# Optimization experiments

Hardware: AMD Instinct MI355X
Metric: run time of the kernel (lower is better)

Reference implementation:

```python
import jax, jax.numpy as jnp
import numpy as np

NUM_HEADS = 12
HEAD_DIM = 64


def setup_inputs() -> dict:
    key = jax.random.key(0)
    ks = jax.random.split(key, 4)
    B, T, C = 2, 2048, 768
    x = jax.random.normal(ks[0], (B, T, C), dtype=jnp.float32)
    attention_mask = jnp.ones((B, 1, 1, T), dtype=jnp.int32)
    W_attn = jax.random.normal(ks[1], (C, 3 * C), dtype=jnp.float32) * 0.02
    b_attn = jnp.zeros((3 * C,), dtype=jnp.float32)
    W_proj = jax.random.normal(ks[2], (C, C), dtype=jnp.float32) * 0.02
    b_proj = jnp.zeros((C,), dtype=jnp.float32)
    return {"x": x, "attention_mask": attention_mask, "W_attn": W_attn,
            "b_attn": b_attn, "W_proj": W_proj, "b_proj": b_proj}


def reference(x, attention_mask, W_attn, b_attn, W_proj, b_proj):
    B, T, C = x.shape
    H, D = NUM_HEADS, HEAD_DIM
    # c_attn (Conv1D): y = x @ W + b -> [B, T, 3C]
    qkv = x @ W_attn + b_attn
    q, k, v = jnp.split(qkv, 3, axis=-1)
    # [B, T, C] -> [B, H, T, D]
    q = q.reshape(B, T, H, D).transpose(0, 2, 1, 3)
    k = k.reshape(B, T, H, D).transpose(0, 2, 1, 3)
    v = v.reshape(B, T, H, D).transpose(0, 2, 1, 3)
    scores = jnp.einsum('bhqd,bhkd->bhqk', q, k) / jnp.sqrt(jnp.float32(D))
    causal = jnp.tril(jnp.ones((T, T), dtype=bool))[None, None]  # [1,1,T,T]
    mask_value = jnp.finfo(scores.dtype).min
    scores = jnp.where(causal, scores, mask_value)
    scores = jnp.where(attention_mask == 0, -jnp.inf, scores)
    probs = jax.nn.softmax(scores, axis=-1)
    attn_out = jnp.einsum('bhqk,bhkd->bhqd', probs, v)
    attn_out = attn_out.transpose(0, 2, 1, 3).reshape(B, T, C)
    return attn_out @ W_proj + b_proj
```

## Files before the change

### kernel.cpp

```cpp
#include <hip/hip_runtime.h>

typedef __attribute__((ext_vector_type(8))) short bf16x8;
typedef __attribute__((ext_vector_type(4))) float f32x4;
typedef __attribute__((ext_vector_type(16))) float f32x16;

#define MFMA16(a, b, c) __builtin_amdgcn_mfma_f32_16x16x32_bf16(a, b, c, 0, 0, 0)
#define MFMA32(a, b, c) __builtin_amdgcn_mfma_f32_32x32x16_bf16(a, b, c, 0, 0, 0)
#define LOG2E 1.4426950408889634f
#define MB2 46.16624868f

#define BB 2
#define TT 2048
#define CC 768
#define HH 12
#define DD 64
#define MM (BB * TT)
#define N1 (3 * CC)
#define BH_STRIDE 131072

static __device__ __forceinline__ unsigned short f2bf(float f) {
  union { float f; unsigned u; } v; v.f = f;
  unsigned r = (v.u + 0x7FFFu + ((v.u >> 16) & 1u)) >> 16;
  return (unsigned short)r;
}

static __device__ __forceinline__ float bf2f(unsigned short s) {
  union { unsigned u; float f; } v; v.u = ((unsigned)s) << 16;
  return v.f;
}

static __device__ __forceinline__ unsigned cvt_pk_bf16(float lo, float hi) {
  unsigned r;
  asm("v_cvt_pk_bf16_f32 %0, %1, %2" : "=v"(r) : "v"(lo), "v"(hi));
  return r;
}

static __device__ __forceinline__ void gload_lds16(const void* g, void* l) {
  __builtin_amdgcn_global_load_lds(
      (const __attribute__((address_space(1))) void*)g,
      (__attribute__((address_space(3))) void*)l, 16, 0, 0);
}

#define PREP_CVT 3072
#define PREP_TR1 1728
#define PREP_TR2 576
__global__ __launch_bounds__(256) void k_prep(
    const float* __restrict__ x, unsigned short* __restrict__ Xb,
    const float* __restrict__ Wa, unsigned short* __restrict__ WaT,
    const float* __restrict__ Wp, unsigned short* __restrict__ WpT,
    const int* __restrict__ mask, unsigned int* __restrict__ mb) {
  __shared__ float tile[32][33];
  const int bid = blockIdx.x;
  const int tid = threadIdx.x;
  if (bid < PREP_CVT) {
    const int i = bid * 256 + tid;
    float4 v = reinterpret_cast<const float4*>(x)[i];
    ushort4 r;
    r.x = f2bf(v.x); r.y = f2bf(v.y); r.z = f2bf(v.z); r.w = f2bf(v.w);
    reinterpret_cast<ushort4*>(Xb)[i] = r;
  } else if (bid < PREP_CVT + PREP_TR1 + PREP_TR2) {
    const bool first = bid < PREP_CVT + PREP_TR1;
    const int b = first ? bid - PREP_CVT : bid - PREP_CVT - PREP_TR1;
    const int nb = first ? 72 : 24;
    const int N = first ? N1 : CC;
    const float* W = first ? Wa : Wp;
    unsigned short* Wt = first ? WaT : WpT;
    const int n0 = (b % nb) * 32, k0 = (b / nb) * 32;
    const int tx = tid & 31, ty = tid >> 5;
#pragma unroll
    for (int i = 0; i < 4; ++i)
      tile[ty + i * 8][tx] = W[(size_t)(k0 + ty + i * 8) * N + n0 + tx];
    __syncthreads();
#pragma unroll
    for (int i = 0; i < 4; ++i)
      Wt[(size_t)(n0 + ty + i * 8) * CC + k0 + tx] = f2bf(tile[tx][ty + i * 8]);
  } else {
    if (tid < 128) {
      unsigned bits = 0;
      const int* p = mask + tid * 32;
#pragma unroll
      for (int j = 0; j < 32; ++j) bits |= (p[j] != 0 ? 1u : 0u) << j;
      mb[tid] = bits;
    }
  }
}

template <int MODE, int BN>
__global__ __launch_bounds__(256) void k_gemm(
    const unsigned short* __restrict__ A, const unsigned short* __restrict__ Bt,
    const float* __restrict__ bias, float* __restrict__ Cout, int N, int K,
    unsigned short* __restrict__ Qb, unsigned short* __restrict__ Kb,
    unsigned short* __restrict__ Vt) {
  constexpr int NI = BN / 32;
  __shared__ __align__(16) unsigned short As[3][128 * 32];
  __shared__ __align__(16) unsigned short Bs[3][BN * 32];
  const int tid = threadIdx.x;
  const int lane = tid & 63;
  const int wid = tid >> 6;
  const int l15 = lane & 15, l4 = lane >> 4;
  const int wr = wid >> 1, wc = wid & 1;
  const int brow = blockIdx.x * 128, bcol = blockIdx.y * BN;

  f32x4 acc[4][NI] = {};

  const int srow = tid >> 2;
  const int usrc = (tid & 3) ^ ((tid >> 3) & 3);
  const unsigned short* gA0 = A + (size_t)(brow + srow) * K + usrc * 8;
  const unsigned short* gA1 = gA0 + (size_t)64 * K;
  const unsigned short* gB0 = Bt + (size_t)(bcol + srow) * K + usrc * 8;
  const unsigned short* gB1 = (BN == 128) ? gB0 + (size_t)64 * K : gB0;
  const int dslot = tid * 8;

  const int NT = K / 32;

#define STAGE(t, buf)                                       \
  do {                                                      \
    const int ko = (t) * 32;                                \
    gload_lds16(gA0 + ko, &As[buf][dslot]);                 \
    gload_lds16(gA1 + ko, &As[buf][dslot + 2048]);          \
    gload_lds16(gB0 + ko, &Bs[buf][dslot]);                 \
    if (BN == 128) gload_lds16(gB1 + ko, &Bs[buf][dslot + 2048]); \
  } while (0)

  const int swz = (l4 ^ ((l15 >> 1) & 3)) * 8;
  const int arow = wr * 64 + l15;
  const int brow2 = wc * (BN / 2) + l15;

  STAGE(0, 0);
  STAGE(1, 1);

  int cur = 0;
  for (int t = 0; t < NT - 1; ++t) {
    if (BN == 128) asm volatile("s_waitcnt vmcnt(4)" ::: "memory");
    else           asm volatile("s_waitcnt vmcnt(3)" ::: "memory");
    __builtin_amdgcn_s_barrier();
    if (t + 2 < NT) {
      int nb = cur + 2; if (nb >= 3) nb -= 3;
      STAGE(t + 2, nb);
    }
    bf16x8 af[4], bfr[NI];
#pragma unroll
    for (int mi = 0; mi < 4; ++mi)
      af[mi] = *reinterpret_cast<const bf16x8*>(&As[cur][(arow + mi * 16) * 32 + swz]);
#pragma unroll
    for (int ni = 0; ni < NI; ++ni)
      bfr[ni] = *reinterpret_cast<const bf16x8*>(&Bs[cur][(brow2 + ni * 16) * 32 + swz]);
#pragma unroll
    for (int mi = 0; mi < 4; ++mi)
#pragma unroll
      for (int ni = 0; ni < NI; ++ni)
        acc[mi][ni] = MFMA16(af[mi], bfr[ni], acc[mi][ni]);
    cur = (cur == 2) ? 0 : cur + 1;
  }
  asm volatile("s_waitcnt vmcnt(0)" ::: "memory");
  __builtin_amdgcn_s_barrier();
  {
    bf16x8 af[4], bfr[NI];
#pragma unroll
    for (int mi = 0; mi < 4; ++mi)
      af[mi] = *reinterpret_cast<const bf16x8*>(&As[cur][(arow + mi * 16) * 32 + swz]);
#pragma unroll
    for (int ni = 0; ni < NI; ++ni)
      bfr[ni] = *reinterpret_cast<const bf16x8*>(&Bs[cur][(brow2 + ni * 16) * 32 + swz]);
#pragma unroll
    for (int mi = 0; mi < 4; ++mi)
#pragma unroll
      for (int ni = 0; ni < NI; ++ni)
        acc[mi][ni] = MFMA16(af[mi], bfr[ni], acc[mi][ni]);
  }
#undef STAGE

#pragma unroll
  for (int mi = 0; mi < 4; ++mi) {
    const int m0 = brow + wr * 64 + mi * 16 + l4 * 4;
#pragma unroll
    for (int ni = 0; ni < NI; ++ni) {
      const int n = bcol + wc * (BN / 2) + ni * 16 + l15;
      const float bv = bias[n];
      if (MODE == 0) {
#pragma unroll
        for (int r = 0; r < 4; ++r)
          Cout[(size_t)(m0 + r) * N + n] = acc[mi][ni][r] + bv;
      } else {
        const int sec = n / CC;
        const int nn = n - sec * CC;
        const int hh = nn >> 6, d = nn & 63;
        const int b = m0 >> 11;
        const int t0 = m0 & 2047;
        const size_t hbase = (size_t)(b * HH + hh) * BH_STRIDE;
        if (sec == 0) {
#pragma unroll
          for (int r = 0; r < 4; ++r) {
            const int t = t0 + r;
            Qb[hbase + ((t >> 5) * 4 + (d >> 4)) * 512 + (t & 31) * 16 + (d & 15)] =
                f2bf((acc[mi][ni][r] + bv) * 0.125f);
          }
        } else if (sec == 1) {
#pragma unroll
          for (int r = 0; r < 4; ++r) {
            const int t = t0 + r;
            Kb[hbase + ((t >> 5) * 4 + (d >> 4)) * 512 + (t & 31) * 16 + (d & 15)] =
                f2bf(acc[mi][ni][r] + bv);
          }
        } else {
          ushort4 pk;
          pk.x = f2bf(acc[mi][ni][0] + bv);
          pk.y = f2bf(acc[mi][ni][1] + bv);
          pk.z = f2bf(acc[mi][ni][2] + bv);
          pk.w = f2bf(acc[mi][ni][3] + bv);
          *reinterpret_cast<ushort4*>(
              &Vt[hbase + ((t0 >> 6) * 4 + ((t0 >> 4) & 3)) * 1024 + d * 16 + (t0 & 15)]) = pk;
        }
      }
    }
  }
}

__device__ __forceinline__ void loadk(bf16x8 (&dst)[2][4], const unsigned short* Kh,
                                      int kv0, int lo) {
  const unsigned short* kp = Kh + (kv0 >> 5) * 2048 + lo;
#pragma unroll
  for (int kg = 0; kg < 2; ++kg)
#pragma unroll
    for (int dg = 0; dg < 4; ++dg)
      dst[kg][dg] = *reinterpret_cast<const bf16x8*>(&kp[kg * 2048 + dg * 512]);
}

__device__ __forceinline__ void attn_tile(
    int kv0, const bf16x8 (&kf)[2][4], uint2 mb, const bf16x8 (&qf)[4],
    const unsigned short* __restrict__ Vh, int q0, int l31, int h, int lo,
    f32x16& o0, f32x16& o1, float& lrow) {
  const unsigned short* vp = Vh + (kv0 >> 6) * 4096 + lo;
  bf16x8 vf0[4], vf1[4];
#pragma unroll
  for (int kc = 0; kc < 4; ++kc) {
    vf0[kc] = *reinterpret_cast<const bf16x8*>(&vp[kc * 1024]);
    vf1[kc] = *reinterpret_cast<const bf16x8*>(&vp[kc * 1024 + 512]);
  }

  f32x16 s0 = {}, s1 = {};
  __builtin_amdgcn_s_setprio(1);
#pragma unroll
  for (int dg = 0; dg < 4; ++dg) s0 = MFMA32(kf[0][dg], qf[dg], s0);
#pragma unroll
  for (int dg = 0; dg < 4; ++dg) s1 = MFMA32(kf[1][dg], qf[dg], s1);
  __builtin_amdgcn_s_setprio(0);

  if ((mb.x & mb.y) != 0xffffffffu) {
#pragma unroll
    for (int r = 0; r < 16; ++r) {
      const int ki = (r & 3) + 8 * (r >> 2) + 4 * h;
      if (!((mb.x >> ki) & 1u)) s0[r] = -1e30f;
      if (!((mb.y >> ki) & 1u)) s1[r] = -1e30f;
    }
  }
  if (kv0 + 63 > q0) {
    const int q = q0 + l31;
#pragma unroll
    for (int r = 0; r < 16; ++r) {
      const int ki = kv0 + (r & 3) + 8 * (r >> 2) + 4 * h;
      if (ki > q) s0[r] = -1e30f;
      if (ki + 32 > q) s1[r] = -1e30f;
    }
  }

#pragma unroll
  for (int r = 0; r < 16; ++r) {
    s0[r] = __builtin_amdgcn_exp2f(__builtin_fmaf(s0[r], LOG2E, -MB2));
    s1[r] = __builtin_amdgcn_exp2f(__builtin_fmaf(s1[r], LOG2E, -MB2));
  }
  float ts[8];
#pragma unroll
  for (int r = 0; r < 8; ++r)
    ts[r] = (s0[2 * r] + s0[2 * r + 1]) + (s1[2 * r] + s1[2 * r + 1]);
  float ps = ((ts[0] + ts[1]) + (ts[2] + ts[3])) + ((ts[4] + ts[5]) + (ts[6] + ts[7]));
  ps += __shfl_xor(ps, 32);
  lrow += ps;

  unsigned pk0[4][2], pk1[4][2];
#pragma unroll
  for (int m = 0; m < 4; ++m)
#pragma unroll
    for (int j = 0; j < 2; ++j) {
      pk0[m][j] = cvt_pk_bf16(s0[4 * m + 2 * j], s0[4 * m + 2 * j + 1]);
      pk1[m][j] = cvt_pk_bf16(s1[4 * m + 2 * j], s1[4 * m + 2 * j + 1]);
    }

#pragma unroll
  for (int kc = 0; kc < 4; ++kc) {
    const unsigned (&pkk)[4][2] = (kc < 2) ? pk0 : pk1;
    const int c1 = (kc & 1) * 2;
    const unsigned v0 = h ? pkk[c1][0] : pkk[c1 + 1][0];
    const unsigned v1 = h ? pkk[c1][1] : pkk[c1 + 1][1];
    const unsigned r0 = (unsigned)__shfl_xor((int)v0, 32);
    const unsigned r1 = (unsigned)__shfl_xor((int)v1, 32);
    union { unsigned u[4]; bf16x8 v; } af;
    af.u[0] = h ? r0 : pkk[c1][0];
    af.u[1] = h ? r1 : pkk[c1][1];
    af.u[2] = h ? pkk[c1 + 1][0] : r0;
    af.u[3] = h ? pkk[c1 + 1][1] : r1;
    __builtin_amdgcn_s_setprio(1);
    o0 = MFMA32(af.v, vf0[kc], o0);
    o1 = MFMA32(af.v, vf1[kc], o1);
    __builtin_amdgcn_s_setprio(0);
  }
}

__global__ __launch_bounds__(256, 2) void k_attn(
    const unsigned short* __restrict__ Q, const unsigned short* __restrict__ Kb,
    const unsigned short* __restrict__ Vt, const unsigned int* __restrict__ mbits,
    unsigned short* __restrict__ pO, float* __restrict__ pL,
    unsigned short* __restrict__ AO) {
  const int tid = threadIdx.x;
  const int lane = tid & 63;
  const int w = tid >> 6;
  const int l31 = lane & 31;
  const int h = lane >> 5;
  const int lo = l31 * 16 + h * 8;
  const int f = blockIdx.x;
  const int xcd = f & 7;
  const int i = f >> 3;
  const int hl = i % 3;
  const int j = i / 3;
  const int bh = xcd * 3 + hl;
  int g, c;
  if (j < 16)      { g = 15 - (j >> 2); c = j & 3; }
  else if (j < 28) { const int u = j - 16; g = 11 - u / 3; c = u % 3; }
  else if (j < 36) { const int u = j - 28; g = 7 - (u >> 1); c = u & 1; }
  else             { g = 3 - (j - 36); c = 0; }
  const int qb = 4 * g + w;
  int cb;
  if (qb < 16)      cb = qb;
  else if (qb < 32) cb = 16 + 2 * (qb - 16);
  else if (qb < 48) cb = 48 + 3 * (qb - 32);
  else              cb = 96 + 4 * (qb - 48);
  const int pidx = bh * 160 + cb + c;

  const int b = bh / HH;
  const int hd = bh - b * HH;
  const int q0 = qb * 32;
  const int nt = qb / 2 + 1;
  const int t0 = c * 8;
  const int t1 = (t0 + 8 < nt) ? t0 + 8 : nt;

  const unsigned short* Qh = Q + (size_t)bh * BH_STRIDE;
  const unsigned short* Kh = Kb + (size_t)bh * BH_STRIDE;
  const unsigned short* Vh = Vt + (size_t)bh * BH_STRIDE;
  const unsigned int* mbp = mbits + b * 64;

  bf16x8 qf[4];
  {
    const unsigned short* qp = Qh + (q0 >> 5) * 2048 + lo;
#pragma unroll
    for (int dg = 0; dg < 4; ++dg)
      qf[dg] = *reinterpret_cast<const bf16x8*>(&qp[dg * 512]);
  }

  f32x16 o0 = {}, o1 = {};
  float lrow = 0.f;

  bf16x8 kfA[2][4], kfB[2][4];
  uint2 mbA, mbB;
  loadk(kfA, Kh, t0 * 64, lo);
  mbA = *reinterpret_cast<const uint2*>(&mbp[t0 * 2]);

  int t = t0;
  while (true) {
    if (t + 1 < t1) {
      loadk(kfB, Kh, (t + 1) * 64, lo);
      mbB = *reinterpret_cast<const uint2*>(&mbp[(t + 1) * 2]);
    }
    attn_tile(t * 64, kfA, mbA, qf, Vh, q0, l31, h, lo, o0, o1, lrow);
    ++t; if (t >= t1) break;
    if (t + 1 < t1) {
      loadk(kfA, Kh, (t + 1) * 64, lo);
      mbA = *reinterpret_cast<const uint2*>(&mbp[(t + 1) * 2]);
    }
    attn_tile(t * 64, kfB, mbB, qf, Vh, q0, l31, h, lo, o0, o1, lrow);
    ++t; if (t >= t1) break;
  }

  if (t0 == 0 && t1 == nt) {
    const float rl = 1.0f / lrow;
#pragma unroll
    for (int r = 0; r < 16; ++r) {
      const int crow = (r & 3) + 8 * (r >> 2) + 4 * h;
      const float rb = __shfl(rl, crow);
      const size_t base = (size_t)(b * TT + q0 + crow) * CC + hd * DD;
      AO[base + l31] = f2bf(o0[r] * rb);
      AO[base + 32 + l31] = f2bf(o1[r] * rb);
    }
  } else {
    unsigned short* po = pO + (size_t)pidx * 2048;
#pragma unroll
    for (int r = 0; r < 16; ++r) {
      const int crow = (r & 3) + 8 * (r >> 2) + 4 * h;
      po[crow * 64 + l31] = f2bf(o0[r]);
      po[crow * 64 + 32 + l31] = f2bf(o1[r]);
    }
    if (lane < 32) {
      pL[pidx * 32 + lane] = lrow;
    }
  }
}

__global__ __launch_bounds__(256) void k_merge(
    const unsigned short* __restrict__ pO, const float* __restrict__ pL,
    unsigned short* __restrict__ AO) {
  const int qb = 16 + blockIdx.x, bh = blockIdx.y;
  const int b = bh / HH, hd = bh - b * HH;
  const int nt = qb / 2 + 1;
  const int nch = (nt + 7) >> 3;
  int cb;
  if (qb < 32)      cb = 16 + 2 * (qb - 16);
  else if (qb < 48) cb = 48 + 3 * (qb - 32);
  else              cb = 96 + 4 * (qb - 48);
  const int p0 = bh * 160 + cb;

  const int q = threadIdx.x >> 3;
  const int d0 = (threadIdx.x & 7) * 8;

  float lst = 0.f;
#pragma unroll
  for (int c = 0; c < 4; ++c)
    if (c < nch) lst += pL[(p0 + c) * 32 + q];
  const float inv = 1.0f / lst;

  float acc[8] = {};
#pragma unroll
  for (int c = 0; c < 4; ++c) {
    if (c < nch) {
      const unsigned short* po = pO + ((size_t)(p0 + c) * 32 + q) * 64 + d0;
      union { uint4 v; unsigned short u[8]; } rd;
      rd.v = *reinterpret_cast<const uint4*>(po);
#pragma unroll
      for (int jj = 0; jj < 8; ++jj) acc[jj] += bf2f(rd.u[jj]);
    }
  }
  union { unsigned short u[8]; uint4 v; } ov;
#pragma unroll
  for (int jj = 0; jj < 8; ++jj) ov.u[jj] = f2bf(acc[jj] * inv);
  *reinterpret_cast<uint4*>(&AO[(size_t)(b * TT + qb * 32 + q) * CC + hd * DD + d0]) = ov.v;
}

extern "C" void kernel_launch(void* const* d_in, const int* in_sizes, int n_in,
                              void* d_out, int out_size, void* d_ws, size_t ws_size,
                              hipStream_t stream) {
  const float* x   = (const float*)d_in[0];
  const int* mask  = (const int*)d_in[1];
  const float* Wa  = (const float*)d_in[2];
  const float* ba  = (const float*)d_in[3];
  const float* Wp  = (const float*)d_in[4];
  const float* bp  = (const float*)d_in[5];
  float* out = (float*)d_out;

  char* ws = (char*)d_ws;
  unsigned short* Xb  = (unsigned short*)(ws);
  unsigned short* WaT = (unsigned short*)(ws + 6291456);
  unsigned short* WpT = (unsigned short*)(ws + 9830400);
  unsigned short* Qb  = (unsigned short*)(ws + 11010048);
  unsigned short* Kb  = (unsigned short*)(ws + 17301504);
  unsigned short* Vt  = (unsigned short*)(ws + 23592960);
  unsigned short* AO  = (unsigned short*)(ws + 29884416);
  unsigned int*   Mb  = (unsigned int*)(ws + 36175872);
  float*          pL  = (float*)(ws + 36667904);
  unsigned short* pO  = (unsigned short*)(ws + 37159424);

  k_prep<<<dim3(PREP_CVT + PREP_TR1 + PREP_TR2 + 1), dim3(256), 0, stream>>>(
      x, Xb, Wa, WaT, Wp, WpT, mask, Mb);

  k_gemm<1, 128><<<dim3(MM / 128, N1 / 128), dim3(256), 0, stream>>>(
      Xb, WaT, ba, nullptr, N1, CC, Qb, Kb, Vt);

  k_attn<<<dim3(960), dim3(256), 0, stream>>>(Qb, Kb, Vt, Mb, pO, pL, AO);
  k_merge<<<dim3(48, BB * HH), dim3(256), 0, stream>>>(pO, pL, AO);

  k_gemm<0, 64><<<dim3(MM / 128, CC / 64), dim3(256), 0, stream>>>(
      AO, WpT, bp, out, CC, CC, nullptr, nullptr, nullptr);
}
```

Measured before the change: 82.58 us.

## Process two 32-row query blocks per wave to reuse K/V fragments

Each attention wave now handles 64 query rows (two 32-row sub-blocks) per KV tile, so every loaded K and V fragment feeds twice the MFMA work. The grid is halved, and the split-KV chunk indexing, partial buffers and merge kernel are rebuilt for 64-row blocks. The double-buffered K prefetch becomes a single buffer reloaded mid-iteration, and the launch-bounds occupancy hint is removed. In exchange, register pressure rises with four accumulators and two Q fragment sets, fewer blocks are resident, and causal masking wastes more work on diagonal tiles.

```diff
diff --git a/kernel.cpp b/kernel.cpp
--- a/kernel.cpp
+++ b/kernel.cpp
@@ -226,26 +226,9 @@
       dst[kg][dg] = *reinterpret_cast<const bf16x8*>(&kp[kg * 2048 + dg * 512]);
 }
 
-__device__ __forceinline__ void attn_tile(
-    int kv0, const bf16x8 (&kf)[2][4], uint2 mb, const bf16x8 (&qf)[4],
-    const unsigned short* __restrict__ Vh, int q0, int l31, int h, int lo,
-    f32x16& o0, f32x16& o1, float& lrow) {
-  const unsigned short* vp = Vh + (kv0 >> 6) * 4096 + lo;
-  bf16x8 vf0[4], vf1[4];
-#pragma unroll
-  for (int kc = 0; kc < 4; ++kc) {
-    vf0[kc] = *reinterpret_cast<const bf16x8*>(&vp[kc * 1024]);
-    vf1[kc] = *reinterpret_cast<const bf16x8*>(&vp[kc * 1024 + 512]);
-  }
-
-  f32x16 s0 = {}, s1 = {};
-  __builtin_amdgcn_s_setprio(1);
-#pragma unroll
-  for (int dg = 0; dg < 4; ++dg) s0 = MFMA32(kf[0][dg], qf[dg], s0);
-#pragma unroll
-  for (int dg = 0; dg < 4; ++dg) s1 = MFMA32(kf[1][dg], qf[dg], s1);
-  __builtin_amdgcn_s_setprio(0);
-
+__device__ __forceinline__ void softmax_pack(
+    f32x16& s0, f32x16& s1, uint2 mb, int kv0, int q0x, int l31, int h,
+    float& lrow, unsigned (&pk0)[4][2], unsigned (&pk1)[4][2]) {
   if ((mb.x & mb.y) != 0xffffffffu) {
 #pragma unroll
     for (int r = 0; r < 16; ++r) {
@@ -254,8 +237,8 @@
       if (!((mb.y >> ki) & 1u)) s1[r] = -1e30f;
     }
   }
-  if (kv0 + 63 > q0) {
-    const int q = q0 + l31;
+  if (kv0 + 63 > q0x) {
+    const int q = q0x + l31;
 #pragma unroll
     for (int r = 0; r < 16; ++r) {
       const int ki = kv0 + (r & 3) + 8 * (r >> 2) + 4 * h;
@@ -263,7 +246,6 @@
       if (ki + 32 > q) s1[r] = -1e30f;
     }
   }
-
 #pragma unroll
   for (int r = 0; r < 16; ++r) {
     s0[r] = __builtin_amdgcn_exp2f(__builtin_fmaf(s0[r], LOG2E, -MB2));
@@ -276,8 +258,6 @@
   float ps = ((ts[0] + ts[1]) + (ts[2] + ts[3])) + ((ts[4] + ts[5]) + (ts[6] + ts[7]));
   ps += __shfl_xor(ps, 32);
   lrow += ps;
-
-  unsigned pk0[4][2], pk1[4][2];
 #pragma unroll
   for (int m = 0; m < 4; ++m)
 #pragma unroll
@@ -285,7 +265,12 @@
       pk0[m][j] = cvt_pk_bf16(s0[4 * m + 2 * j], s0[4 * m + 2 * j + 1]);
       pk1[m][j] = cvt_pk_bf16(s1[4 * m + 2 * j], s1[4 * m + 2 * j + 1]);
     }
-
+}
+
+__device__ __forceinline__ void pv_acc(
+    const unsigned (&pk0)[4][2], const unsigned (&pk1)[4][2],
+    const bf16x8 (&vf0)[4], const bf16x8 (&vf1)[4], int h,
+    f32x16& o0, f32x16& o1) {
 #pragma unroll
   for (int kc = 0; kc < 4; ++kc) {
     const unsigned (&pkk)[4][2] = (kc < 2) ? pk0 : pk1;
@@ -306,7 +291,7 @@
   }
 }
 
-__global__ __launch_bounds__(256, 2) void k_attn(
+__global__ void k_attn(
     const unsigned short* __restrict__ Q, const unsigned short* __restrict__ Kb,
     const unsigned short* __restrict__ Vt, const unsigned int* __restrict__ mbits,
     unsigned short* __restrict__ pO, float* __restrict__ pL,
@@ -323,23 +308,27 @@
   const int hl = i % 3;
   const int j = i / 3;
   const int bh = xcd * 3 + hl;
-  int g, c;
-  if (j < 16)      { g = 15 - (j >> 2); c = j & 3; }
-  else if (j < 28) { const int u = j - 16; g = 11 - u / 3; c = u % 3; }
-  else if (j < 36) { const int u = j - 28; g = 7 - (u >> 1); c = u & 1; }
-  else             { g = 3 - (j - 36); c = 0; }
-  const int qb = 4 * g + w;
+  int G, c;
+  if (j < 4)        { G = 7; c = j; }
+  else if (j < 8)   { G = 6; c = j - 4; }
+  else if (j < 11)  { G = 5; c = j - 8; }
+  else if (j < 14)  { G = 4; c = j - 11; }
+  else if (j < 16)  { G = 3; c = j - 14; }
+  else if (j < 18)  { G = 2; c = j - 16; }
+  else if (j == 18) { G = 1; c = 0; }
+  else              { G = 0; c = 0; }
+  const int k = 4 * G + w;
   int cb;
-  if (qb < 16)      cb = qb;
-  else if (qb < 32) cb = 16 + 2 * (qb - 16);
-  else if (qb < 48) cb = 48 + 3 * (qb - 32);
-  else              cb = 96 + 4 * (qb - 48);
-  const int pidx = bh * 160 + cb + c;
+  if (k < 8)       cb = k;
+  else if (k < 16) cb = 8 + 2 * (k - 8);
+  else if (k < 24) cb = 24 + 3 * (k - 16);
+  else             cb = 48 + 4 * (k - 24);
+  const int pidx = bh * 80 + cb + c;
 
   const int b = bh / HH;
   const int hd = bh - b * HH;
-  const int q0 = qb * 32;
-  const int nt = qb / 2 + 1;
+  const int q0 = k * 64;
+  const int nt = k + 1;
   const int t0 = c * 8;
   const int t1 = (t0 + 8 < nt) ? t0 + 8 : nt;
 
@@ -348,58 +337,86 @@
   const unsigned short* Vh = Vt + (size_t)bh * BH_STRIDE;
   const unsigned int* mbp = mbits + b * 64;
 
-  bf16x8 qf[4];
+  bf16x8 qfA[4], qfB[4];
   {
-    const unsigned short* qp = Qh + (q0 >> 5) * 2048 + lo;
-#pragma unroll
-    for (int dg = 0; dg < 4; ++dg)
-      qf[dg] = *reinterpret_cast<const bf16x8*>(&qp[dg * 512]);
-  }
-
-  f32x16 o0 = {}, o1 = {};
-  float lrow = 0.f;
-
-  bf16x8 kfA[2][4], kfB[2][4];
-  uint2 mbA, mbB;
-  loadk(kfA, Kh, t0 * 64, lo);
-  mbA = *reinterpret_cast<const uint2*>(&mbp[t0 * 2]);
-
-  int t = t0;
-  while (true) {
-    if (t + 1 < t1) {
-      loadk(kfB, Kh, (t + 1) * 64, lo);
-      mbB = *reinterpret_cast<const uint2*>(&mbp[(t + 1) * 2]);
-    }
-    attn_tile(t * 64, kfA, mbA, qf, Vh, q0, l31, h, lo, o0, o1, lrow);
-    ++t; if (t >= t1) break;
-    if (t + 1 < t1) {
-      loadk(kfA, Kh, (t + 1) * 64, lo);
-      mbA = *reinterpret_cast<const uint2*>(&mbp[(t + 1) * 2]);
-    }
-    attn_tile(t * 64, kfB, mbB, qf, Vh, q0, l31, h, lo, o0, o1, lrow);
-    ++t; if (t >= t1) break;
+    const unsigned short* qp = Qh + (size_t)2 * k * 2048 + lo;
+#pragma unroll
+    for (int dg = 0; dg < 4; ++dg) {
+      qfA[dg] = *reinterpret_cast<const bf16x8*>(&qp[dg * 512]);
+      qfB[dg] = *reinterpret_cast<const bf16x8*>(&qp[2048 + dg * 512]);
+    }
+  }
+
+  f32x16 oA0 = {}, oA1 = {}, oB0 = {}, oB1 = {};
+  float lA = 0.f, lB = 0.f;
+
+  bf16x8 kf[2][4];
+  loadk(kf, Kh, t0 * 64, lo);
+
+  for (int t = t0; t < t1; ++t) {
+    const unsigned short* vp = Vh + t * 4096 + lo;
+    bf16x8 vf0[4], vf1[4];
+#pragma unroll
+    for (int kc = 0; kc < 4; ++kc) {
+      vf0[kc] = *reinterpret_cast<const bf16x8*>(&vp[kc * 1024]);
+      vf1[kc] = *reinterpret_cast<const bf16x8*>(&vp[kc * 1024 + 512]);
+    }
+    const uint2 mbt = *reinterpret_cast<const uint2*>(&mbp[t * 2]);
+
+    f32x16 s0 = {}, s1 = {};
+    __builtin_amdgcn_s_setprio(1);
+#pragma unroll
+    for (int dg = 0; dg < 4; ++dg) s0 = MFMA32(kf[0][dg], qfA[dg], s0);
+#pragma unroll
+    for (int dg = 0; dg < 4; ++dg) s1 = MFMA32(kf[1][dg], qfA[dg], s1);
+    __builtin_amdgcn_s_setprio(0);
+    unsigned pkA0[4][2], pkA1[4][2];
+    softmax_pack(s0, s1, mbt, t * 64, q0, l31, h, lA, pkA0, pkA1);
+
+    f32x16 u0 = {}, u1 = {};
+    __builtin_amdgcn_s_setprio(1);
+#pragma unroll
+    for (int dg = 0; dg < 4; ++dg) u0 = MFMA32(kf[0][dg], qfB[dg], u0);
+#pragma unroll
+    for (int dg = 0; dg < 4; ++dg) u1 = MFMA32(kf[1][dg], qfB[dg], u1);
+    __builtin_amdgcn_s_setprio(0);
+    unsigned pkB0[4][2], pkB1[4][2];
+    softmax_pack(u0, u1, mbt, t * 64, q0 + 32, l31, h, lB, pkB0, pkB1);
+
+    if (t + 1 < t1) loadk(kf, Kh, (t + 1) * 64, lo);
+
+    pv_acc(pkA0, pkA1, vf0, vf1, h, oA0, oA1);
+    pv_acc(pkB0, pkB1, vf0, vf1, h, oB0, oB1);
   }
 
   if (t0 == 0 && t1 == nt) {
-    const float rl = 1.0f / lrow;
+    const float rlA = 1.0f / lA;
+    const float rlB = 1.0f / lB;
 #pragma unroll
     for (int r = 0; r < 16; ++r) {
       const int crow = (r & 3) + 8 * (r >> 2) + 4 * h;
-      const float rb = __shfl(rl, crow);
-      const size_t base = (size_t)(b * TT + q0 + crow) * CC + hd * DD;
-      AO[base + l31] = f2bf(o0[r] * rb);
-      AO[base + 32 + l31] = f2bf(o1[r] * rb);
+      const float rbA = __shfl(rlA, crow);
+      const float rbB = __shfl(rlB, crow);
+      const size_t baseA = (size_t)(b * TT + q0 + crow) * CC + hd * DD;
+      const size_t baseB = (size_t)(b * TT + q0 + 32 + crow) * CC + hd * DD;
+      AO[baseA + l31] = f2bf(oA0[r] * rbA);
+      AO[baseA + 32 + l31] = f2bf(oA1[r] * rbA);
+      AO[baseB + l31] = f2bf(oB0[r] * rbB);
+      AO[baseB + 32 + l31] = f2bf(oB1[r] * rbB);
     }
   } else {
-    unsigned short* po = pO + (size_t)pidx * 2048;
+    unsigned short* po = pO + (size_t)pidx * 4096;
 #pragma unroll
     for (int r = 0; r < 16; ++r) {
       const int crow = (r & 3) + 8 * (r >> 2) + 4 * h;
-      po[crow * 64 + l31] = f2bf(o0[r]);
-      po[crow * 64 + 32 + l31] = f2bf(o1[r]);
+      po[crow * 64 + l31] = f2bf(oA0[r]);
+      po[crow * 64 + 32 + l31] = f2bf(oA1[r]);
+      po[(32 + crow) * 64 + l31] = f2bf(oB0[r]);
+      po[(32 + crow) * 64 + 32 + l31] = f2bf(oB1[r]);
     }
     if (lane < 32) {
-      pL[pidx * 32 + lane] = lrow;
+      pL[pidx * 64 + lane] = lA;
+      pL[pidx * 64 + 32 + lane] = lB;
     }
   }
 }
@@ -407,40 +424,49 @@
 __global__ __launch_bounds__(256) void k_merge(
     const unsigned short* __restrict__ pO, const float* __restrict__ pL,
     unsigned short* __restrict__ AO) {
-  const int qb = 16 + blockIdx.x, bh = blockIdx.y;
+  const int kk = 8 + blockIdx.x;
+  const int bh = blockIdx.y;
   const int b = bh / HH, hd = bh - b * HH;
-  const int nt = qb / 2 + 1;
-  const int nch = (nt + 7) >> 3;
+  const int nch = (kk + 8) >> 3;
   int cb;
-  if (qb < 32)      cb = 16 + 2 * (qb - 16);
-  else if (qb < 48) cb = 48 + 3 * (qb - 32);
-  else              cb = 96 + 4 * (qb - 48);
-  const int p0 = bh * 160 + cb;
-
-  const int q = threadIdx.x >> 3;
-  const int d0 = (threadIdx.x & 7) * 8;
+  if (kk < 16)      cb = 8 + 2 * (kk - 8);
+  else if (kk < 24) cb = 24 + 3 * (kk - 16);
+  else              cb = 48 + 4 * (kk - 24);
+  const int p0 = bh * 80 + cb;
+
+  const int q = threadIdx.x >> 2;
+  const int d0 = (threadIdx.x & 3) * 16;
 
   float lst = 0.f;
 #pragma unroll
   for (int c = 0; c < 4; ++c)
-    if (c < nch) lst += pL[(p0 + c) * 32 + q];
+    if (c < nch) lst += pL[(p0 + c) * 64 + q];
   const float inv = 1.0f / lst;
 
-  float acc[8] = {};
+  float acc[16] = {};
 #pragma unroll
   for (int c = 0; c < 4; ++c) {
     if (c < nch) {
-      const unsigned short* po = pO + ((size_t)(p0 + c) * 32 + q) * 64 + d0;
-      union { uint4 v; unsigned short u[8]; } rd;
-      rd.v = *reinterpret_cast<const uint4*>(po);
-#pragma unroll
-      for (int jj = 0; jj < 8; ++jj) acc[jj] += bf2f(rd.u[jj]);
-    }
-  }
-  union { unsigned short u[8]; uint4 v; } ov;
-#pragma unroll
-  for (int jj = 0; jj < 8; ++jj) ov.u[jj] = f2bf(acc[jj] * inv);
-  *reinterpret_cast<uint4*>(&AO[(size_t)(b * TT + qb * 32 + q) * CC + hd * DD + d0]) = ov.v;
+      const unsigned short* po = pO + (size_t)(p0 + c) * 4096 + q * 64 + d0;
+      union { uint4 v; unsigned short u[8]; } rd0, rd1;
+      rd0.v = *reinterpret_cast<const uint4*>(po);
+      rd1.v = *reinterpret_cast<const uint4*>(po + 8);
+#pragma unroll
+      for (int jj = 0; jj < 8; ++jj) {
+        acc[jj] += bf2f(rd0.u[jj]);
+        acc[8 + jj] += bf2f(rd1.u[jj]);
+      }
+    }
+  }
+  union { unsigned short u[8]; uint4 v; } ov0, ov1;
+#pragma unroll
+  for (int jj = 0; jj < 8; ++jj) {
+    ov0.u[jj] = f2bf(acc[jj] * inv);
+    ov1.u[jj] = f2bf(acc[8 + jj] * inv);
+  }
+  unsigned short* dst = &AO[(size_t)(b * TT + kk * 64 + q) * CC + hd * DD + d0];
+  *reinterpret_cast<uint4*>(dst) = ov0.v;
+  *reinterpret_cast<uint4*>(dst + 8) = ov1.v;
 }
 
 extern "C" void kernel_launch(void* const* d_in, const int* in_sizes, int n_in,
@@ -472,8 +498,8 @@
   k_gemm<1, 128><<<dim3(MM / 128, N1 / 128), dim3(256), 0, stream>>>(
       Xb, WaT, ba, nullptr, N1, CC, Qb, Kb, Vt);
 
-  k_attn<<<dim3(960), dim3(256), 0, stream>>>(Qb, Kb, Vt, Mb, pO, pL, AO);
-  k_merge<<<dim3(48, BB * HH), dim3(256), 0, stream>>>(pO, pL, AO);
+  k_attn<<<dim3(480), dim3(256), 0, stream>>>(Qb, Kb, Vt, Mb, pO, pL, AO);
+  k_merge<<<dim3(24, BB * HH), dim3(256), 0, stream>>>(pO, pL, AO);
 
   k_gemm<0, 64><<<dim3(MM / 128, CC / 64), dim3(256), 0, stream>>>(
       AO, WpT, bp, out, CC, CC, nullptr, nullptr, nullptr);
```

After: 256.7 us. +210.9%, slower.

## Fuse split-KV merge into attention kernel via atomic last-block reduction

Applied to the files above, without the earlier changes.

Removes the separate merge kernel launch. Each attention block writes its partial output and row sums, then increments a per-(head, query-group) counter, and the last arriving block does the merge for all four query blocks of that group. The counters are zeroed in the prep kernel. This saves a kernel launch and its gap, at the cost of thread fences, an atomic per block, and merge work serialized at the end of some attention blocks.

```diff
diff --git a/kernel.cpp b/kernel.cpp
--- a/kernel.cpp
+++ b/kernel.cpp
@@ -41,6 +41,13 @@
       (__attribute__((address_space(3))) void*)l, 16, 0, 0);
 }
 
+static __device__ __forceinline__ int cbof(int qb) {
+  if (qb < 16) return qb;
+  if (qb < 32) return 16 + 2 * (qb - 16);
+  if (qb < 48) return 48 + 3 * (qb - 32);
+  return 96 + 4 * (qb - 48);
+}
+
 #define PREP_CVT 3072
 #define PREP_TR1 1728
 #define PREP_TR2 576
@@ -48,7 +55,8 @@
     const float* __restrict__ x, unsigned short* __restrict__ Xb,
     const float* __restrict__ Wa, unsigned short* __restrict__ WaT,
     const float* __restrict__ Wp, unsigned short* __restrict__ WpT,
-    const int* __restrict__ mask, unsigned int* __restrict__ mb) {
+    const int* __restrict__ mask, unsigned int* __restrict__ mb,
+    unsigned int* __restrict__ cnt) {
   __shared__ float tile[32][33];
   const int bid = blockIdx.x;
   const int tid = threadIdx.x;
@@ -82,6 +90,7 @@
       for (int j = 0; j < 32; ++j) bits |= (p[j] != 0 ? 1u : 0u) << j;
       mb[tid] = bits;
     }
+    for (int z = tid; z < 384; z += 256) cnt[z] = 0;
   }
 }
 
@@ -310,7 +319,8 @@
     const unsigned short* __restrict__ Q, const unsigned short* __restrict__ Kb,
     const unsigned short* __restrict__ Vt, const unsigned int* __restrict__ mbits,
     unsigned short* __restrict__ pO, float* __restrict__ pL,
-    unsigned short* __restrict__ AO) {
+    unsigned short* __restrict__ AO, unsigned int* __restrict__ cnt) {
+  __shared__ unsigned s_old;
   const int tid = threadIdx.x;
   const int lane = tid & 63;
   const int w = tid >> 6;
@@ -328,13 +338,9 @@
   else if (j < 28) { const int u = j - 16; g = 11 - u / 3; c = u % 3; }
   else if (j < 36) { const int u = j - 28; g = 7 - (u >> 1); c = u & 1; }
   else             { g = 3 - (j - 36); c = 0; }
+  const int nc = (g >= 12) ? 4 : (g >= 8) ? 3 : (g >= 4) ? 2 : 1;
   const int qb = 4 * g + w;
-  int cb;
-  if (qb < 16)      cb = qb;
-  else if (qb < 32) cb = 16 + 2 * (qb - 16);
-  else if (qb < 48) cb = 48 + 3 * (qb - 32);
-  else              cb = 96 + 4 * (qb - 48);
-  const int pidx = bh * 160 + cb + c;
+  const int pidx = bh * 160 + cbof(qb) + c;
 
   const int b = bh / HH;
   const int hd = bh - b * HH;
@@ -380,7 +386,7 @@
     ++t; if (t >= t1) break;
   }
 
-  if (t0 == 0 && t1 == nt) {
+  if (nc == 1) {
     const float rl = 1.0f / lrow;
 #pragma unroll
     for (int r = 0; r < 16; ++r) {
@@ -390,7 +396,10 @@
       AO[base + l31] = f2bf(o0[r] * rb);
       AO[base + 32 + l31] = f2bf(o1[r] * rb);
     }
-  } else {
+    return;
+  }
+
+  {
     unsigned short* po = pO + (size_t)pidx * 2048;
 #pragma unroll
     for (int r = 0; r < 16; ++r) {
@@ -402,45 +411,36 @@
       pL[pidx * 32 + lane] = lrow;
     }
   }
-}
-
-__global__ __launch_bounds__(256) void k_merge(
-    const unsigned short* __restrict__ pO, const float* __restrict__ pL,
-    unsigned short* __restrict__ AO) {
-  const int qb = 16 + blockIdx.x, bh = blockIdx.y;
-  const int b = bh / HH, hd = bh - b * HH;
-  const int nt = qb / 2 + 1;
-  const int nch = (nt + 7) >> 3;
-  int cb;
-  if (qb < 32)      cb = 16 + 2 * (qb - 16);
-  else if (qb < 48) cb = 48 + 3 * (qb - 32);
-  else              cb = 96 + 4 * (qb - 48);
-  const int p0 = bh * 160 + cb;
-
-  const int q = threadIdx.x >> 3;
-  const int d0 = (threadIdx.x & 7) * 8;
-
-  float lst = 0.f;
-#pragma unroll
-  for (int c = 0; c < 4; ++c)
-    if (c < nch) lst += pL[(p0 + c) * 32 + q];
-  const float inv = 1.0f / lst;
-
-  float acc[8] = {};
-#pragma unroll
-  for (int c = 0; c < 4; ++c) {
-    if (c < nch) {
-      const unsigned short* po = pO + ((size_t)(p0 + c) * 32 + q) * 64 + d0;
+  __threadfence();
+  __syncthreads();
+  if (tid == 0) s_old = atomicAdd(&cnt[bh * 16 + g], 1u);
+  __syncthreads();
+  if (s_old != (unsigned)(nc - 1)) return;
+  __threadfence();
+
+  const int q = tid >> 3;
+  const int d0 = (tid & 7) * 8;
+#pragma unroll
+  for (int w2 = 0; w2 < 4; ++w2) {
+    const int qb2 = 4 * g + w2;
+    const int p0 = bh * 160 + cbof(qb2);
+    float lst = 0.f;
+    for (int cc = 0; cc < nc; ++cc) lst += pL[(p0 + cc) * 32 + q];
+    const float inv = 1.0f / lst;
+    float acc[8] = {};
+    for (int cc = 0; cc < nc; ++cc) {
+      const unsigned short* po = pO + ((size_t)(p0 + cc) * 32 + q) * 64 + d0;
       union { uint4 v; unsigned short u[8]; } rd;
       rd.v = *reinterpret_cast<const uint4*>(po);
 #pragma unroll
       for (int jj = 0; jj < 8; ++jj) acc[jj] += bf2f(rd.u[jj]);
     }
-  }
-  union { unsigned short u[8]; uint4 v; } ov;
-#pragma unroll
-  for (int jj = 0; jj < 8; ++jj) ov.u[jj] = f2bf(acc[jj] * inv);
-  *reinterpret_cast<uint4*>(&AO[(size_t)(b * TT + qb * 32 + q) * CC + hd * DD + d0]) = ov.v;
+    union { unsigned short u[8]; uint4 v; } ov;
+#pragma unroll
+    for (int jj = 0; jj < 8; ++jj) ov.u[jj] = f2bf(acc[jj] * inv);
+    *reinterpret_cast<uint4*>(
+        &AO[(size_t)(b * TT + qb2 * 32 + q) * CC + hd * DD + d0]) = ov.v;
+  }
 }
 
 extern "C" void kernel_launch(void* const* d_in, const int* in_sizes, int n_in,
@@ -465,15 +465,15 @@
   unsigned int*   Mb  = (unsigned int*)(ws + 36175872);
   float*          pL  = (float*)(ws + 36667904);
   unsigned short* pO  = (unsigned short*)(ws + 37159424);
+  unsigned int*   Cn  = (unsigned int*)(ws + 52888064);
 
   k_prep<<<dim3(PREP_CVT + PREP_TR1 + PREP_TR2 + 1), dim3(256), 0, stream>>>(
-      x, Xb, Wa, WaT, Wp, WpT, mask, Mb);
+      x, Xb, Wa, WaT, Wp, WpT, mask, Mb, Cn);
 
   k_gemm<1, 128><<<dim3(MM / 128, N1 / 128), dim3(256), 0, stream>>>(
       Xb, WaT, ba, nullptr, N1, CC, Qb, Kb, Vt);
 
-  k_attn<<<dim3(960), dim3(256), 0, stream>>>(Qb, Kb, Vt, Mb, pO, pL, AO);
-  k_merge<<<dim3(48, BB * HH), dim3(256), 0, stream>>>(pO, pL, AO);
+  k_attn<<<dim3(960), dim3(256), 0, stream>>>(Qb, Kb, Vt, Mb, pO, pL, AO, Cn);
 
   k_gemm<0, 64><<<dim3(MM / 128, CC / 64), dim3(256), 0, stream>>>(
       AO, WpT, bp, out, CC, CC, nullptr, nullptr, nullptr);
```

Result: slower. 213.2 us (+158.2%).
